# Performance work log

Hardware: AMD Instinct MI355X
Metric: run time of the kernel (lower is better)

Reference implementation:

```python
import jax, jax.numpy as jnp
import numpy as np

B, S, T, D, H, DF, E = 16, 1024, 512, 512, 8, 2048, 4
DH = D // H
EPS = 1e-5


def setup_inputs() -> dict:
    key = jax.random.key(0)
    ks = iter(jax.random.split(key, 64))

    def nrm(shape, scale=0.02):
        return jax.random.normal(next(ks), shape, dtype=jnp.float32) * scale

    inp = {
        "x": jax.random.normal(next(ks), (B, S, D), dtype=jnp.float32),
        "cross": jax.random.normal(next(ks), (B, T, D), dtype=jnp.float32),
    }
    for p in ("sa", "ca"):
        for w in ("wq", "wk", "wv", "wo"):
            inp[f"{p}_{w}"] = nrm((D, D))
            inp[f"{p}_b{w[1]}"] = jnp.zeros((D,), jnp.float32)
    inp["gate_w"] = nrm((D, E))
    inp["gate_b"] = jnp.zeros((E,), jnp.float32)
    inp["exp_w1"] = nrm((E, D, DF))
    inp["exp_b1"] = jnp.zeros((E, DF), jnp.float32)
    inp["exp_w2"] = nrm((E, DF, D))
    inp["exp_b2"] = jnp.zeros((E, D), jnp.float32)
    for i in (1, 2, 3):
        inp[f"n{i}_g"] = jnp.ones((D,), jnp.float32)
        inp[f"n{i}_b"] = jnp.zeros((D,), jnp.float32)
    return inp


def layer_norm(x, g, b):
    m = x.mean(-1, keepdims=True)
    v = x.var(-1, keepdims=True)
    return (x - m) * jax.lax.rsqrt(v + EPS) * g + b


def mha(q_in, kv_in, wq, bq, wk, bk, wv, bv, wo, bo, causal):
    Bq, Sq, _ = q_in.shape
    Sk = kv_in.shape[1]
    q = (q_in @ wq + bq).reshape(Bq, Sq, H, DH)
    k = (kv_in @ wk + bk).reshape(Bq, Sk, H, DH)
    v = (kv_in @ wv + bv).reshape(Bq, Sk, H, DH)
    scores = jnp.einsum('bshd,bthd->bhst', q, k) / jnp.sqrt(jnp.float32(DH))
    if causal:
        mask = jnp.tril(jnp.ones((Sq, Sk), dtype=bool))
        scores = jnp.where(mask, scores, jnp.float32(-1e9))
    attn = jax.nn.softmax(scores, axis=-1)
    out = jnp.einsum('bhst,bthd->bshd', attn, v).reshape(Bq, Sq, D)
    return out @ wo + bo


def moe_ffn(x, gw, gb, w1, b1, w2, b2):
    gates = jax.nn.softmax(x @ gw + gb, axis=-1)            # [B,S,E]
    h = jax.nn.relu(jnp.einsum('bsd,edf->bsef', x, w1) + b1)  # [B,S,E,DF]
    yo = jnp.einsum('bsef,efd->bsed', h, w2) + b2            # [B,S,E,D]
    y = jnp.einsum('bse,bsed->bsd', gates, yo)
    imp = gates.mean((0, 1))                                 # importance per expert
    aux = jnp.float32(E) * jnp.sum(imp * imp)                # load-balance penalty
    return y, aux


def reference(x, cross,
              sa_wq, sa_bq, sa_wk, sa_bk, sa_wv, sa_bv, sa_wo, sa_bo,
              ca_wq, ca_bq, ca_wk, ca_bk, ca_wv, ca_bv, ca_wo, ca_bo,
              gate_w, gate_b, exp_w1, exp_b1, exp_w2, exp_b2,
              n1_g, n1_b, n2_g, n2_b, n3_g, n3_b):
    # dropout is identity in eval mode
    x = x + mha(x, x, sa_wq, sa_bq, sa_wk, sa_bk, sa_wv, sa_bv, sa_wo, sa_bo, causal=True)
    x = layer_norm(x, n1_g, n1_b)
    x = x + mha(x, cross, ca_wq, ca_bq, ca_wk, ca_bk, ca_wv, ca_bv, ca_wo, ca_bo, causal=False)
    x = layer_norm(x, n2_g, n2_b)
    y, aux_loss = moe_ffn(x, gate_w, gate_b, exp_w1, exp_b1, exp_w2, exp_b2)
    out = layer_norm(x + y, n3_g, n3_b)
    return out, aux_loss
```

## Files before the change

kernel.cpp:

```cpp
#include <hip/hip_runtime.h>
#include <stdint.h>
#include <stddef.h>

typedef unsigned short bf16u;
typedef __attribute__((ext_vector_type(8))) short short8;
typedef __attribute__((ext_vector_type(4))) float f32x4;

__device__ __forceinline__ bf16u f2bf(float f) {
  union { float f; unsigned u; } v; v.f = f;
  unsigned r = v.u + 0x7FFFu + ((v.u >> 16) & 1u);
  return (bf16u)(r >> 16);
}

#define GL16(g, l) __builtin_amdgcn_global_load_lds( \
    (const __attribute__((address_space(1))) unsigned int*)(g), \
    (__attribute__((address_space(3))) unsigned int*)(l), 16, 0, 0)

enum { EPI_BF16 = 0, EPI_RELU_GATE = 1, EPI_VT = 2, EPI_RES = 3, EPI_ACC = 4 };

template<int EPI>
__global__ __launch_bounds__(256, 2) void gemm_k(
    const bf16u* __restrict__ A, const bf16u* __restrict__ BT,
    const float* __restrict__ bias, const float* __restrict__ res,
    const float* __restrict__ gates,
    bf16u* __restrict__ outb, float* __restrict__ outf,
    int M, int N, int K, int slog, int egate, int firste)
{
  __shared__ bf16u Ab[2][128 * 32];
  __shared__ bf16u Bb[2][128 * 32];
  const int tid = threadIdx.x, lane = tid & 63, w = tid >> 6;
  const int wm = w >> 1, wn = w & 1;
  const int nbt = N >> 7;
  const int mt = blockIdx.x / nbt, nt = blockIdx.x - mt * nbt;
  const int bm = mt << 7, bn = nt << 7;

  const int srow = lane >> 2;
  const int scol = (lane & 3) << 3;
  const bf16u* ap0 = A + (size_t)(bm + w * 16 + srow) * K + scol;
  const bf16u* ap1 = ap0 + (size_t)64 * K;
  const bf16u* bp0 = BT + (size_t)(bn + w * 16 + srow) * K + scol;
  const bf16u* bp1 = bp0 + (size_t)64 * K;

  f32x4 acc[4][4] = {};
  const int NT = K >> 5;

  GL16(ap0, &Ab[0][w * 512]);
  GL16(ap1, &Ab[0][(4 + w) * 512]);
  GL16(bp0, &Bb[0][w * 512]);
  GL16(bp1, &Bb[0][(4 + w) * 512]);
  __syncthreads();

  const int rl = lane & 15, kg = (lane >> 4) << 3;
  int cur = 0;
  for (int kt = 0; kt < NT; ++kt) {
    if (kt + 1 < NT) {
      const int ko = (kt + 1) << 5;
      const int nb = cur ^ 1;
      GL16(ap0 + ko, &Ab[nb][w * 512]);
      GL16(ap1 + ko, &Ab[nb][(4 + w) * 512]);
      GL16(bp0 + ko, &Bb[nb][w * 512]);
      GL16(bp1 + ko, &Bb[nb][(4 + w) * 512]);
    }
    short8 af[4], bfv[4];
    #pragma unroll
    for (int i = 0; i < 4; ++i)
      af[i] = *(const short8*)&Ab[cur][(wm * 64 + i * 16 + rl) * 32 + kg];
    #pragma unroll
    for (int j = 0; j < 4; ++j)
      bfv[j] = *(const short8*)&Bb[cur][(wn * 64 + j * 16 + rl) * 32 + kg];
    #pragma unroll
    for (int i = 0; i < 4; ++i)
      #pragma unroll
      for (int j = 0; j < 4; ++j)
        acc[i][j] = __builtin_amdgcn_mfma_f32_16x16x32_bf16(af[i], bfv[j], acc[i][j], 0, 0, 0);
    __syncthreads();
    cur ^= 1;
  }

  const int r0 = bm + wm * 64, c0 = bn + wn * 64;
  const int rsub = (lane >> 4) << 2;
  #pragma unroll
  for (int j = 0; j < 4; ++j) {
    const int col = c0 + j * 16 + rl;
    const float bs = bias ? bias[col] : 0.f;
    #pragma unroll
    for (int i = 0; i < 4; ++i) {
      const f32x4 v = acc[i][j];
      #pragma unroll
      for (int jj = 0; jj < 4; ++jj) {
        const int row = r0 + i * 16 + rsub + jj;
        float val = v[jj] + bs;
        if (EPI == EPI_BF16) {
          outb[(size_t)row * N + col] = f2bf(val);
        } else if (EPI == EPI_RELU_GATE) {
          const float g = gates[(size_t)row * 4 + egate];
          outb[(size_t)row * N + col] = f2bf(g * (val > 0.f ? val : 0.f));
        } else if (EPI == EPI_VT) {
          const int b_ = row >> slog, t_ = row & ((1 << slog) - 1);
          outb[(((size_t)(b_ * 8 + (col >> 6)) << 6) + (size_t)(col & 63)) * ((size_t)1 << slog) + t_] = f2bf(val);
        } else if (EPI == EPI_RES) {
          outf[(size_t)row * N + col] = res[(size_t)row * N + col] + val;
        } else {
          const size_t oi = (size_t)row * N + col;
          outf[oi] = firste ? val : (outf[oi] + val);
        }
      }
    }
  }
}

template<bool CAUSAL>
__global__ __launch_bounds__(256, 4) void attn_k(
    const bf16u* __restrict__ Q, const bf16u* __restrict__ Kg,
    const bf16u* __restrict__ VT, bf16u* __restrict__ O,
    int Sq, int Sk)
{
  __shared__ bf16u Kl[2][64 * 64];
  __shared__ bf16u Vl[2][64 * 64];
  __shared__ bf16u Pl[64 * 64];
  const int nqt = Sq >> 6;
  const int bh = blockIdx.x / nqt, qt = blockIdx.x - bh * nqt;
  const int b = bh >> 3, h = bh & 7;
  const int tid = threadIdx.x, lane = tid & 63, w = tid >> 6;
  const int rl = lane & 15, g4 = lane >> 4;

  const int qrow = qt * 64 + w * 16 + rl;
  const bf16u* qp = Q + (size_t)(b * Sq + qrow) * 512 + h * 64 + g4 * 8;
  const short8 qf0 = *(const short8*)qp;
  const short8 qf1 = *(const short8*)(qp + 32);

  f32x4 oacc[4] = {};
  float ml = -1e30f, ll = 0.f;
  const int KT = CAUSAL ? (qt + 1) : (Sk >> 6);

  const int str = tid >> 2, stc = tid & 3;
  const int sw_st = (str & 7) << 4;
  const bf16u* kq = Kg + (size_t)(b * Sk + str) * 512 + h * 64 + stc * 8;
  const bf16u* vq = VT + (size_t)(bh * 64 + str) * Sk + stc * 8;
  const int lo0 = str * 128 + ((stc * 16) ^ sw_st);
  const int lo1 = str * 128 + ((stc * 16 + 64) ^ sw_st);

  const int qr = w * 16 + rl;
  char* const pbase = (char*)Pl + qr * 128;
  const int swq = (qr & 7) << 4;

  {
    const short8 k0 = *(const short8*)kq;
    const short8 k1 = *(const short8*)(kq + 32);
    const short8 v0 = *(const short8*)vq;
    const short8 v1 = *(const short8*)(vq + 32);
    *(short8*)((char*)Kl[0] + lo0) = k0;
    *(short8*)((char*)Kl[0] + lo1) = k1;
    *(short8*)((char*)Vl[0] + lo0) = v0;
    *(short8*)((char*)Vl[0] + lo1) = v1;
  }
  __syncthreads();

  int cur = 0;
  for (int kt = 0; kt < KT; ++kt) {
    short8 nk0, nk1, nv0, nv1;
    const bool pre = (kt + 1 < KT);
    if (pre) {
      const bf16u* ks = kq + (size_t)(kt + 1) * 64 * 512;
      const bf16u* vs = vq + (kt + 1) * 64;
      nk0 = *(const short8*)ks;
      nk1 = *(const short8*)(ks + 32);
      nv0 = *(const short8*)vs;
      nv1 = *(const short8*)(vs + 32);
    }

    const bf16u* Kc = Kl[cur];
    const bf16u* Vc = Vl[cur];
    f32x4 st[4] = {};
    #pragma unroll
    for (int mi = 0; mi < 4; ++mi) {
      const int kr = mi * 16 + rl;
      const char* kb_ = (const char*)Kc + kr * 128;
      const int sw = (kr & 7) << 4;
      const short8 kf0 = *(const short8*)(kb_ + ((g4 * 16) ^ sw));
      const short8 kf1 = *(const short8*)(kb_ + ((g4 * 16 + 64) ^ sw));
      st[mi] = __builtin_amdgcn_mfma_f32_16x16x32_bf16(kf0, qf0, st[mi], 0, 0, 0);
      st[mi] = __builtin_amdgcn_mfma_f32_16x16x32_bf16(kf1, qf1, st[mi], 0, 0, 0);
    }

    const float SC = 0.125f * 1.44269504f;
    float sv[16];
    float pm = -1e30f;
    if (CAUSAL && kt == qt) {
      const int qg = qt * 64 + qr;
      #pragma unroll
      for (int mi = 0; mi < 4; ++mi)
        #pragma unroll
        for (int jj = 0; jj < 4; ++jj) {
          float s = st[mi][jj] * SC;
          const int kgi = kt * 64 + mi * 16 + g4 * 4 + jj;
          if (kgi > qg) s = -1e30f;
          sv[mi * 4 + jj] = s;
          pm = fmaxf(pm, s);
        }
    } else {
      #pragma unroll
      for (int mi = 0; mi < 4; ++mi)
        #pragma unroll
        for (int jj = 0; jj < 4; ++jj) {
          const float s = st[mi][jj] * SC;
          sv[mi * 4 + jj] = s;
          pm = fmaxf(pm, s);
        }
    }
    pm = fmaxf(pm, __shfl_xor(pm, 16));
    pm = fmaxf(pm, __shfl_xor(pm, 32));
    const float mnew = fmaxf(ml, pm);
    const float alpha = exp2f(ml - mnew);
    float ps = 0.f;
    bf16u pb[16];
    #pragma unroll
    for (int ii = 0; ii < 16; ++ii) {
      const float p = exp2f(sv[ii] - mnew);
      ps += p;
      pb[ii] = f2bf(p);
    }
    ps += __shfl_xor(ps, 16);
    ps += __shfl_xor(ps, 32);
    ll = ll * alpha + ps;
    ml = mnew;

    #pragma unroll
    for (int jj = 0; jj < 4; ++jj) {
      const float aj = __shfl(alpha, g4 * 4 + jj);
      #pragma unroll
      for (int ni = 0; ni < 4; ++ni) oacc[ni][jj] *= aj;
    }

    #pragma unroll
    for (int mi = 0; mi < 4; ++mi) {
      #pragma unroll
      for (int jp = 0; jp < 2; ++jp) {
        const unsigned pk = (unsigned)pb[mi * 4 + jp * 2] | ((unsigned)pb[mi * 4 + jp * 2 + 1] << 16);
        const int kx2 = mi * 32 + g4 * 8 + jp * 4;
        *(unsigned*)(pbase + (kx2 ^ swq)) = pk;
      }
    }
    asm volatile("s_waitcnt lgkmcnt(0)" ::: "memory");
    #pragma unroll
    for (int ks = 0; ks < 2; ++ks) {
      const short8 pf = *(const short8*)(pbase + ((g4 * 16 + ks * 64) ^ swq));
      #pragma unroll
      for (int ni = 0; ni < 4; ++ni) {
        const int vr = ni * 16 + rl;
        const short8 vf = *(const short8*)((const char*)Vc + vr * 128 + ((g4 * 16 + ks * 64) ^ ((vr & 7) << 4)));
        oacc[ni] = __builtin_amdgcn_mfma_f32_16x16x32_bf16(pf, vf, oacc[ni], 0, 0, 0);
      }
    }

    __syncthreads();
    if (pre) {
      const int nb = cur ^ 1;
      *(short8*)((char*)Kl[nb] + lo0) = nk0;
      *(short8*)((char*)Kl[nb] + lo1) = nk1;
      *(short8*)((char*)Vl[nb] + lo0) = nv0;
      *(short8*)((char*)Vl[nb] + lo1) = nv1;
      __syncthreads();
    }
    cur ^= 1;
  }

  #pragma unroll
  for (int jj = 0; jj < 4; ++jj) {
    const float lj = __shfl(ll, g4 * 4 + jj);
    const float inv = 1.f / lj;
    const int row = qt * 64 + w * 16 + g4 * 4 + jj;
    #pragma unroll
    for (int ni = 0; ni < 4; ++ni)
      O[(size_t)(b * Sq + row) * 512 + h * 64 + ni * 16 + rl] = f2bf(oacc[ni][jj] * inv);
  }
}

template<bool ADD, bool BOUT>
__global__ __launch_bounds__(256, 4) void ln_k(
    const float* __restrict__ X, const float* __restrict__ Y,
    const float* __restrict__ gam, const float* __restrict__ bet,
    float* __restrict__ outf, bf16u* __restrict__ outb)
{
  const int row = blockIdx.x * 4 + (threadIdx.x >> 6);
  const int lane = threadIdx.x & 63;
  const float* xp = X + (size_t)row * 512 + lane * 8;
  float v[8];
  {
    const float4 t0 = *(const float4*)xp;
    const float4 t1 = *(const float4*)(xp + 4);
    v[0] = t0.x; v[1] = t0.y; v[2] = t0.z; v[3] = t0.w;
    v[4] = t1.x; v[5] = t1.y; v[6] = t1.z; v[7] = t1.w;
  }
  if (ADD) {
    const float* yp = Y + (size_t)row * 512 + lane * 8;
    const float4 t0 = *(const float4*)yp;
    const float4 t1 = *(const float4*)(yp + 4);
    v[0] += t0.x; v[1] += t0.y; v[2] += t0.z; v[3] += t0.w;
    v[4] += t1.x; v[5] += t1.y; v[6] += t1.z; v[7] += t1.w;
  }
  float s = 0.f, q = 0.f;
  #pragma unroll
  for (int i = 0; i < 8; ++i) { s += v[i]; q += v[i] * v[i]; }
  #pragma unroll
  for (int off = 1; off < 64; off <<= 1) {
    s += __shfl_xor(s, off);
    q += __shfl_xor(q, off);
  }
  const float mean = s * (1.f / 512.f);
  const float var = q * (1.f / 512.f) - mean * mean;
  const float rs = rsqrtf(var + 1e-5f);
  float o[8];
  #pragma unroll
  for (int i = 0; i < 8; ++i) {
    const float g = gam[lane * 8 + i], bb = bet[lane * 8 + i];
    o[i] = (v[i] - mean) * rs * g + bb;
  }
  float* op = outf + (size_t)row * 512 + lane * 8;
  *(float4*)op = make_float4(o[0], o[1], o[2], o[3]);
  *(float4*)(op + 4) = make_float4(o[4], o[5], o[6], o[7]);
  if (BOUT) {
    union { bf16u u[8]; short8 v8; } pk;
    #pragma unroll
    for (int i = 0; i < 8; ++i) pk.u[i] = f2bf(o[i]);
    *(short8*)(outb + (size_t)row * 512 + lane * 8) = pk.v8;
  }
}

__global__ __launch_bounds__(256, 4) void ln_final_k(
    const float* __restrict__ X, const float* __restrict__ Y,
    const float* __restrict__ gates, const float* __restrict__ b2,
    const float* __restrict__ gam, const float* __restrict__ bet,
    float* __restrict__ outf)
{
  const int row = blockIdx.x * 4 + (threadIdx.x >> 6);
  const int lane = threadIdx.x & 63;
  const float4 gv4 = *(const float4*)(gates + (size_t)row * 4);
  float v[8];
  {
    const float* xp = X + (size_t)row * 512 + lane * 8;
    const float* yp = Y + (size_t)row * 512 + lane * 8;
    const float4 t0 = *(const float4*)xp;
    const float4 t1 = *(const float4*)(xp + 4);
    const float4 u0 = *(const float4*)yp;
    const float4 u1 = *(const float4*)(yp + 4);
    v[0] = t0.x + u0.x; v[1] = t0.y + u0.y; v[2] = t0.z + u0.z; v[3] = t0.w + u0.w;
    v[4] = t1.x + u1.x; v[5] = t1.y + u1.y; v[6] = t1.z + u1.z; v[7] = t1.w + u1.w;
  }
  #pragma unroll
  for (int e = 0; e < 4; ++e) {
    const float ge = e == 0 ? gv4.x : e == 1 ? gv4.y : e == 2 ? gv4.z : gv4.w;
    const float4 b0 = *(const float4*)(b2 + e * 512 + lane * 8);
    const float4 b1 = *(const float4*)(b2 + e * 512 + lane * 8 + 4);
    v[0] += ge * b0.x; v[1] += ge * b0.y; v[2] += ge * b0.z; v[3] += ge * b0.w;
    v[4] += ge * b1.x; v[5] += ge * b1.y; v[6] += ge * b1.z; v[7] += ge * b1.w;
  }
  float s = 0.f, q = 0.f;
  #pragma unroll
  for (int i = 0; i < 8; ++i) { s += v[i]; q += v[i] * v[i]; }
  #pragma unroll
  for (int off = 1; off < 64; off <<= 1) {
    s += __shfl_xor(s, off);
    q += __shfl_xor(q, off);
  }
  const float mean = s * (1.f / 512.f);
  const float var = q * (1.f / 512.f) - mean * mean;
  const float rs = rsqrtf(var + 1e-5f);
  float* op = outf + (size_t)row * 512 + lane * 8;
  float o[8];
  #pragma unroll
  for (int i = 0; i < 8; ++i)
    o[i] = (v[i] - mean) * rs * gam[lane * 8 + i] + bet[lane * 8 + i];
  *(float4*)op = make_float4(o[0], o[1], o[2], o[3]);
  *(float4*)(op + 4) = make_float4(o[4], o[5], o[6], o[7]);
}

__global__ __launch_bounds__(256, 4) void gate_k(
    const float* __restrict__ X, const float* __restrict__ gw,
    const float* __restrict__ gb, float* __restrict__ gates,
    float* __restrict__ imp)
{
  __shared__ float sh[4];
  const int tid = threadIdx.x;
  if (tid < 4) sh[tid] = 0.f;
  __syncthreads();
  const int row = blockIdx.x * 4 + (tid >> 6);
  const int lane = tid & 63;
  const float* xr = X + (size_t)row * 512;
  float a0 = 0.f, a1 = 0.f, a2 = 0.f, a3 = 0.f;
  for (int d = lane; d < 512; d += 64) {
    const float xv = xr[d];
    const float4 wv = *(const float4*)(gw + d * 4);
    a0 += xv * wv.x; a1 += xv * wv.y; a2 += xv * wv.z; a3 += xv * wv.w;
  }
  #pragma unroll
  for (int off = 1; off < 64; off <<= 1) {
    a0 += __shfl_xor(a0, off); a1 += __shfl_xor(a1, off);
    a2 += __shfl_xor(a2, off); a3 += __shfl_xor(a3, off);
  }
  if (lane == 0) {
    a0 += gb[0]; a1 += gb[1]; a2 += gb[2]; a3 += gb[3];
    const float m = fmaxf(fmaxf(a0, a1), fmaxf(a2, a3));
    const float e0 = exp2f((a0 - m) * 1.44269504f);
    const float e1 = exp2f((a1 - m) * 1.44269504f);
    const float e2 = exp2f((a2 - m) * 1.44269504f);
    const float e3 = exp2f((a3 - m) * 1.44269504f);
    const float inv = 1.f / (e0 + e1 + e2 + e3);
    float* gr = gates + (size_t)row * 4;
    const float g0 = e0 * inv, g1 = e1 * inv, g2 = e2 * inv, g3 = e3 * inv;
    gr[0] = g0; gr[1] = g1; gr[2] = g2; gr[3] = g3;
    atomicAdd(&sh[0], g0); atomicAdd(&sh[1], g1);
    atomicAdd(&sh[2], g2); atomicAdd(&sh[3], g3);
  }
  __syncthreads();
  if (tid < 4) atomicAdd(&imp[tid], sh[tid]);
}

__global__ void aux_k(const float* __restrict__ imp, float* __restrict__ out) {
  if (threadIdx.x == 0 && blockIdx.x == 0) {
    float s = 0.f;
    #pragma unroll
    for (int e = 0; e < 4; ++e) { const float v = imp[e] * (1.f / 16384.f); s += v * v; }
    out[0] = 4.f * s;
  }
}

__global__ __launch_bounds__(256, 4) void conv_k(const float* __restrict__ in, bf16u* __restrict__ out) {
  const size_t i = ((size_t)blockIdx.x * 256 + threadIdx.x) * 8;
  const float4 a = *(const float4*)(in + i);
  const float4 b = *(const float4*)(in + i + 4);
  union { bf16u u[8]; short8 v; } pk;
  pk.u[0] = f2bf(a.x); pk.u[1] = f2bf(a.y); pk.u[2] = f2bf(a.z); pk.u[3] = f2bf(a.w);
  pk.u[4] = f2bf(b.x); pk.u[5] = f2bf(b.y); pk.u[6] = f2bf(b.z); pk.u[7] = f2bf(b.w);
  *(short8*)(out + i) = pk.v;
}

__global__ __launch_bounds__(256, 4) void trans_k(
    const float* __restrict__ W, bf16u* __restrict__ WT, int K, int N)
{
  __shared__ float t[32][33];
  const int tx = threadIdx.x & 31, ty = threadIdx.x >> 5;
  const int n0 = blockIdx.x * 32, k0 = blockIdx.y * 32;
  #pragma unroll
  for (int i = 0; i < 4; ++i)
    t[ty + i * 8][tx] = W[(size_t)(k0 + ty + i * 8) * N + n0 + tx];
  __syncthreads();
  #pragma unroll
  for (int i = 0; i < 4; ++i)
    WT[(size_t)(n0 + ty + i * 8) * K + k0 + tx] = f2bf(t[tx][ty + i * 8]);
}

extern "C" void kernel_launch(void* const* d_in, const int* in_sizes, int n_in,
                              void* d_out, int out_size, void* d_ws, size_t ws_size,
                              hipStream_t stream)
{
  const int B = 16, S = 1024, T = 512, D = 512, DF = 2048, E = 4;
  const int M = B * S;
  const int Mc = B * T;
  (void)in_sizes; (void)n_in; (void)out_size; (void)ws_size;

  const float* x      = (const float*)d_in[0];
  const float* cross  = (const float*)d_in[1];
  const float* gate_w = (const float*)d_in[18];
  const float* gate_b = (const float*)d_in[19];
  const float* exp_w1 = (const float*)d_in[20];
  const float* exp_b1 = (const float*)d_in[21];
  const float* exp_w2 = (const float*)d_in[22];
  const float* exp_b2 = (const float*)d_in[23];

  char* p = (char*)d_ws;
  auto alloc = [&](size_t bytes) -> char* {
    char* r = p;
    p += (bytes + 255) & ~(size_t)255;
    return r;
  };
  bf16u* xb    = (bf16u*)alloc((size_t)M * D * 2);
  bf16u* crb   = (bf16u*)alloc((size_t)Mc * D * 2);
  bf16u* wT    = (bf16u*)alloc((size_t)8 * D * D * 2);
  bf16u* w1T   = (bf16u*)alloc((size_t)E * DF * D * 2);
  bf16u* w2T   = (bf16u*)alloc((size_t)E * D * DF * 2);
  bf16u* qb    = (bf16u*)alloc((size_t)M * D * 2);
  bf16u* kb    = (bf16u*)alloc((size_t)M * D * 2);
  bf16u* vTb   = (bf16u*)alloc((size_t)M * D * 2);
  bf16u* ao    = (bf16u*)alloc((size_t)M * D * 2);
  float* xf    = (float*)alloc((size_t)M * D * 4);
  bf16u* x2b   = (bf16u*)alloc((size_t)M * D * 2);
  float* gates = (float*)alloc((size_t)M * 4 * 4);
  float* imp   = (float*)alloc(256);
  bf16u* hbuf  = (bf16u*)alloc((size_t)M * DF * 2);
  float* y     = (float*)alloc((size_t)M * D * 4);

  hipMemsetAsync(imp, 0, 32, stream);
  conv_k<<<(M * D) / 2048, 256, 0, stream>>>(x, xb);
  conv_k<<<(Mc * D) / 2048, 256, 0, stream>>>(cross, crb);
  for (int i = 0; i < 8; ++i)
    trans_k<<<dim3(D / 32, D / 32), 256, 0, stream>>>((const float*)d_in[2 + 2 * i], wT + (size_t)i * D * D, D, D);
  for (int e = 0; e < E; ++e)
    trans_k<<<dim3(DF / 32, D / 32), 256, 0, stream>>>(exp_w1 + (size_t)e * D * DF, w1T + (size_t)e * DF * D, D, DF);
  for (int e = 0; e < E; ++e)
    trans_k<<<dim3(D / 32, DF / 32), 256, 0, stream>>>(exp_w2 + (size_t)e * DF * D, w2T + (size_t)e * D * DF, DF, D);

  const int gMD  = (M / 128) * (D / 128);
  const int gMcD = (Mc / 128) * (D / 128);
  const int gMDF = (M / 128) * (DF / 128);

  gemm_k<EPI_BF16><<<gMD, 256, 0, stream>>>(xb, wT + 0 * (size_t)D * D, (const float*)d_in[3], nullptr, nullptr, qb, nullptr, M, D, D, 0, 0, 0);
  gemm_k<EPI_BF16><<<gMD, 256, 0, stream>>>(xb, wT + 1 * (size_t)D * D, (const float*)d_in[5], nullptr, nullptr, kb, nullptr, M, D, D, 0, 0, 0);
  gemm_k<EPI_VT><<<gMD, 256, 0, stream>>>(xb, wT + 2 * (size_t)D * D, (const float*)d_in[7], nullptr, nullptr, vTb, nullptr, M, D, D, 10, 0, 0);
  attn_k<true><<<B * 8 * (S / 64), 256, 0, stream>>>(qb, kb, vTb, ao, S, S);
  gemm_k<EPI_RES><<<gMD, 256, 0, stream>>>(ao, wT + 3 * (size_t)D * D, (const float*)d_in[9], x, nullptr, nullptr, xf, M, D, D, 0, 0, 0);
  ln_k<false, true><<<M / 4, 256, 0, stream>>>(xf, nullptr, (const float*)d_in[24], (const float*)d_in[25], xf, x2b);

  gemm_k<EPI_BF16><<<gMD, 256, 0, stream>>>(x2b, wT + 4 * (size_t)D * D, (const float*)d_in[11], nullptr, nullptr, qb, nullptr, M, D, D, 0, 0, 0);
  gemm_k<EPI_BF16><<<gMcD, 256, 0, stream>>>(crb, wT + 5 * (size_t)D * D, (const float*)d_in[13], nullptr, nullptr, kb, nullptr, Mc, D, D, 0, 0, 0);
  gemm_k<EPI_VT><<<gMcD, 256, 0, stream>>>(crb, wT + 6 * (size_t)D * D, (const float*)d_in[15], nullptr, nullptr, vTb, nullptr, Mc, D, D, 9, 0, 0);
  attn_k<false><<<B * 8 * (S / 64), 256, 0, stream>>>(qb, kb, vTb, ao, S, T);
  gemm_k<EPI_RES><<<gMD, 256, 0, stream>>>(ao, wT + 7 * (size_t)D * D, (const float*)d_in[17], xf, nullptr, nullptr, xf, M, D, D, 0, 0, 0);
  ln_k<false, true><<<M / 4, 256, 0, stream>>>(xf, nullptr, (const float*)d_in[26], (const float*)d_in[27], xf, x2b);

  gate_k<<<M / 4, 256, 0, stream>>>(xf, gate_w, gate_b, gates, imp);
  aux_k<<<1, 64, 0, stream>>>(imp, (float*)d_out + (size_t)M * D);
  for (int e = 0; e < E; ++e) {
    gemm_k<EPI_RELU_GATE><<<gMDF, 256, 0, stream>>>(x2b, w1T + (size_t)e * DF * D, exp_b1 + (size_t)e * DF, nullptr, gates, hbuf, nullptr, M, DF, D, 0, e, 0);
    gemm_k<EPI_ACC><<<gMD, 256, 0, stream>>>(hbuf, w2T + (size_t)e * D * DF, nullptr, nullptr, nullptr, nullptr, y, M, D, DF, 0, 0, e == 0 ? 1 : 0);
  }
  ln_final_k<<<M / 4, 256, 0, stream>>>(xf, y, gates, exp_b2, (const float*)d_in[28], (const float*)d_in[29], (float*)d_out);
}
```

Before: 1.010 ms.

## Process 128 query rows per attention block, read K/V from global, remap block ids

The attention kernel now handles two 64-row query tiles per block, sharing each K and V fragment between both tiles. It drops the LDS double-buffered K/V staging and block-wide barriers, loading K and V fragments straight from global memory, which relies on cache hits instead. It also packs probabilities with v_cvt_pk_bf16_f32. Both the GEMM and attention kernels remap block ids across 8 groups, presumably to spread neighbouring tiles over XCDs for better L2 locality. In exchange, register pressure rises (launch bounds lowered to 3 blocks) and the attention grid is halved.

```diff
diff --git a/kernel.cpp b/kernel.cpp
--- a/kernel.cpp
+++ b/kernel.cpp
@@ -30,8 +30,10 @@
   __shared__ bf16u Bb[2][128 * 32];
   const int tid = threadIdx.x, lane = tid & 63, w = tid >> 6;
   const int wm = w >> 1, wn = w & 1;
+  const int cpx = gridDim.x >> 3;
+  const int bid = (blockIdx.x & 7) * cpx + (blockIdx.x >> 3);
   const int nbt = N >> 7;
-  const int mt = blockIdx.x / nbt, nt = blockIdx.x - mt * nbt;
+  const int mt = bid / nbt, nt = bid - mt * nbt;
   const int bm = mt << 7, bn = nt << 7;
 
   const int srow = lane >> 2;
@@ -109,170 +111,135 @@
   }
 }
 
+#define SOFTMAX_G(stv, mlv, llv, oaccv, pbX, DOMASK, QG)                     \
+  {                                                                          \
+    float sv[16]; float pm = -1e30f;                                         \
+    _Pragma("unroll")                                                        \
+    for (int mi = 0; mi < 4; ++mi) {                                         \
+      _Pragma("unroll")                                                      \
+      for (int jj = 0; jj < 4; ++jj) {                                       \
+        float s_ = stv[mi][jj] * SC;                                         \
+        if (DOMASK) {                                                        \
+          const int kgi = kt * 64 + mi * 16 + g4 * 4 + jj;                   \
+          if (kgi > (QG)) s_ = -1e30f;                                       \
+        }                                                                    \
+        sv[mi * 4 + jj] = s_; pm = fmaxf(pm, s_);                            \
+      }                                                                      \
+    }                                                                        \
+    pm = fmaxf(pm, __shfl_xor(pm, 16));                                      \
+    pm = fmaxf(pm, __shfl_xor(pm, 32));                                      \
+    const float mnew = fmaxf(mlv, pm);                                       \
+    const float alpha = exp2f(mlv - mnew);                                   \
+    float ps = 0.f;                                                          \
+    _Pragma("unroll")                                                        \
+    for (int mi = 0; mi < 4; ++mi) {                                         \
+      const float p0_ = exp2f(sv[mi * 4 + 0] - mnew);                        \
+      const float p1_ = exp2f(sv[mi * 4 + 1] - mnew);                        \
+      const float p2_ = exp2f(sv[mi * 4 + 2] - mnew);                        \
+      const float p3_ = exp2f(sv[mi * 4 + 3] - mnew);                        \
+      ps += (p0_ + p1_) + (p2_ + p3_);                                       \
+      unsigned w0_, w1_;                                                     \
+      asm("v_cvt_pk_bf16_f32 %0, %1, %2" : "=v"(w0_) : "v"(p0_), "v"(p1_)); \
+      asm("v_cvt_pk_bf16_f32 %0, %1, %2" : "=v"(w1_) : "v"(p2_), "v"(p3_)); \
+      *(unsigned*)(pbX + ((mi * 32 + g4 * 8 + 0) ^ swq)) = w0_;              \
+      *(unsigned*)(pbX + ((mi * 32 + g4 * 8 + 4) ^ swq)) = w1_;              \
+    }                                                                        \
+    ps += __shfl_xor(ps, 16);                                                \
+    ps += __shfl_xor(ps, 32);                                                \
+    llv = llv * alpha + ps; mlv = mnew;                                      \
+    _Pragma("unroll")                                                        \
+    for (int jj = 0; jj < 4; ++jj) {                                         \
+      const float aj = __shfl(alpha, g4 * 4 + jj);                           \
+      _Pragma("unroll")                                                      \
+      for (int ni = 0; ni < 4; ++ni) oaccv[ni][jj] *= aj;                    \
+    }                                                                        \
+  }
+
 template<bool CAUSAL>
-__global__ __launch_bounds__(256, 4) void attn_k(
+__global__ __launch_bounds__(256, 3) void attn_k(
     const bf16u* __restrict__ Q, const bf16u* __restrict__ Kg,
     const bf16u* __restrict__ VT, bf16u* __restrict__ O,
     int Sq, int Sk)
 {
-  __shared__ bf16u Kl[2][64 * 64];
-  __shared__ bf16u Vl[2][64 * 64];
-  __shared__ bf16u Pl[64 * 64];
-  const int nqt = Sq >> 6;
-  const int bh = blockIdx.x / nqt, qt = blockIdx.x - bh * nqt;
+  __shared__ bf16u Pl[128 * 64];
+  const int nqt = Sq >> 7;
+  const int cpx = gridDim.x >> 3;
+  const int bid = (blockIdx.x & 7) * cpx + (blockIdx.x >> 3);
+  const int bh = bid / nqt, qt = bid - bh * nqt;
   const int b = bh >> 3, h = bh & 7;
   const int tid = threadIdx.x, lane = tid & 63, w = tid >> 6;
   const int rl = lane & 15, g4 = lane >> 4;
 
-  const int qrow = qt * 64 + w * 16 + rl;
-  const bf16u* qp = Q + (size_t)(b * Sq + qrow) * 512 + h * 64 + g4 * 8;
-  const short8 qf0 = *(const short8*)qp;
-  const short8 qf1 = *(const short8*)(qp + 32);
-
-  f32x4 oacc[4] = {};
-  float ml = -1e30f, ll = 0.f;
-  const int KT = CAUSAL ? (qt + 1) : (Sk >> 6);
-
-  const int str = tid >> 2, stc = tid & 3;
-  const int sw_st = (str & 7) << 4;
-  const bf16u* kq = Kg + (size_t)(b * Sk + str) * 512 + h * 64 + stc * 8;
-  const bf16u* vq = VT + (size_t)(bh * 64 + str) * Sk + stc * 8;
-  const int lo0 = str * 128 + ((stc * 16) ^ sw_st);
-  const int lo1 = str * 128 + ((stc * 16 + 64) ^ sw_st);
-
   const int qr = w * 16 + rl;
-  char* const pbase = (char*)Pl + qr * 128;
+  const int qbase = qt * 128;
+
+  const bf16u* qp0 = Q + (size_t)(b * Sq + qbase + qr) * 512 + h * 64 + g4 * 8;
+  const bf16u* qp1 = qp0 + (size_t)64 * 512;
+  const short8 qa0 = *(const short8*)qp0;
+  const short8 qa1 = *(const short8*)(qp0 + 32);
+  const short8 qc0 = *(const short8*)qp1;
+  const short8 qc1 = *(const short8*)(qp1 + 32);
+
+  f32x4 oacc0[4] = {}, oacc1[4] = {};
+  float ml0 = -1e30f, ll0 = 0.f, ml1 = -1e30f, ll1 = 0.f;
+  const int KT = CAUSAL ? (2 * qt + 2) : (Sk >> 6);
+
+  const bf16u* kbase = Kg + (size_t)b * Sk * 512 + h * 64;
+  const bf16u* vbase = VT + (size_t)bh * 64 * Sk;
+
+  char* const pb0 = (char*)Pl + qr * 128;
+  char* const pb1 = (char*)Pl + (64 + qr) * 128;
   const int swq = (qr & 7) << 4;
-
-  {
-    const short8 k0 = *(const short8*)kq;
-    const short8 k1 = *(const short8*)(kq + 32);
-    const short8 v0 = *(const short8*)vq;
-    const short8 v1 = *(const short8*)(vq + 32);
-    *(short8*)((char*)Kl[0] + lo0) = k0;
-    *(short8*)((char*)Kl[0] + lo1) = k1;
-    *(short8*)((char*)Vl[0] + lo0) = v0;
-    *(short8*)((char*)Vl[0] + lo1) = v1;
-  }
-  __syncthreads();
-
-  int cur = 0;
+  const float SC = 0.125f * 1.44269504f;
+
   for (int kt = 0; kt < KT; ++kt) {
-    short8 nk0, nk1, nv0, nv1;
-    const bool pre = (kt + 1 < KT);
-    if (pre) {
-      const bf16u* ks = kq + (size_t)(kt + 1) * 64 * 512;
-      const bf16u* vs = vq + (kt + 1) * 64;
-      nk0 = *(const short8*)ks;
-      nk1 = *(const short8*)(ks + 32);
-      nv0 = *(const short8*)vs;
-      nv1 = *(const short8*)(vs + 32);
+    const bool mask0 = CAUSAL && (kt == 2 * qt);
+    const bool skip0 = CAUSAL && (kt == 2 * qt + 1);
+    const bool mask1 = CAUSAL && (kt == 2 * qt + 1);
+
+    f32x4 st0[4] = {}, st1[4] = {};
+    #pragma unroll
+    for (int mi = 0; mi < 4; ++mi) {
+      const bf16u* kp = kbase + (size_t)(kt * 64 + mi * 16 + rl) * 512 + g4 * 8;
+      const short8 kf0 = *(const short8*)kp;
+      const short8 kf1 = *(const short8*)(kp + 32);
+      if (!skip0) {
+        st0[mi] = __builtin_amdgcn_mfma_f32_16x16x32_bf16(kf0, qa0, st0[mi], 0, 0, 0);
+        st0[mi] = __builtin_amdgcn_mfma_f32_16x16x32_bf16(kf1, qa1, st0[mi], 0, 0, 0);
+      }
+      st1[mi] = __builtin_amdgcn_mfma_f32_16x16x32_bf16(kf0, qc0, st1[mi], 0, 0, 0);
+      st1[mi] = __builtin_amdgcn_mfma_f32_16x16x32_bf16(kf1, qc1, st1[mi], 0, 0, 0);
     }
 
-    const bf16u* Kc = Kl[cur];
-    const bf16u* Vc = Vl[cur];
-    f32x4 st[4] = {};
-    #pragma unroll
-    for (int mi = 0; mi < 4; ++mi) {
-      const int kr = mi * 16 + rl;
-      const char* kb_ = (const char*)Kc + kr * 128;
-      const int sw = (kr & 7) << 4;
-      const short8 kf0 = *(const short8*)(kb_ + ((g4 * 16) ^ sw));
-      const short8 kf1 = *(const short8*)(kb_ + ((g4 * 16 + 64) ^ sw));
-      st[mi] = __builtin_amdgcn_mfma_f32_16x16x32_bf16(kf0, qf0, st[mi], 0, 0, 0);
-      st[mi] = __builtin_amdgcn_mfma_f32_16x16x32_bf16(kf1, qf1, st[mi], 0, 0, 0);
-    }
-
-    const float SC = 0.125f * 1.44269504f;
-    float sv[16];
-    float pm = -1e30f;
-    if (CAUSAL && kt == qt) {
-      const int qg = qt * 64 + qr;
+    if (!skip0) SOFTMAX_G(st0, ml0, ll0, oacc0, pb0, mask0, qbase + qr);
+    SOFTMAX_G(st1, ml1, ll1, oacc1, pb1, mask1, qbase + 64 + qr);
+
+    asm volatile("s_waitcnt lgkmcnt(0)" ::: "memory");
+
+    #pragma unroll
+    for (int ks = 0; ks < 2; ++ks) {
+      const short8 pf0 = *(const short8*)(pb0 + ((g4 * 16 + ks * 64) ^ swq));
+      const short8 pf1 = *(const short8*)(pb1 + ((g4 * 16 + ks * 64) ^ swq));
       #pragma unroll
-      for (int mi = 0; mi < 4; ++mi)
-        #pragma unroll
-        for (int jj = 0; jj < 4; ++jj) {
-          float s = st[mi][jj] * SC;
-          const int kgi = kt * 64 + mi * 16 + g4 * 4 + jj;
-          if (kgi > qg) s = -1e30f;
-          sv[mi * 4 + jj] = s;
-          pm = fmaxf(pm, s);
-        }
-    } else {
-      #pragma unroll
-      for (int mi = 0; mi < 4; ++mi)
-        #pragma unroll
-        for (int jj = 0; jj < 4; ++jj) {
-          const float s = st[mi][jj] * SC;
-          sv[mi * 4 + jj] = s;
-          pm = fmaxf(pm, s);
-        }
-    }
-    pm = fmaxf(pm, __shfl_xor(pm, 16));
-    pm = fmaxf(pm, __shfl_xor(pm, 32));
-    const float mnew = fmaxf(ml, pm);
-    const float alpha = exp2f(ml - mnew);
-    float ps = 0.f;
-    bf16u pb[16];
-    #pragma unroll
-    for (int ii = 0; ii < 16; ++ii) {
-      const float p = exp2f(sv[ii] - mnew);
-      ps += p;
-      pb[ii] = f2bf(p);
-    }
-    ps += __shfl_xor(ps, 16);
-    ps += __shfl_xor(ps, 32);
-    ll = ll * alpha + ps;
-    ml = mnew;
-
-    #pragma unroll
-    for (int jj = 0; jj < 4; ++jj) {
-      const float aj = __shfl(alpha, g4 * 4 + jj);
-      #pragma unroll
-      for (int ni = 0; ni < 4; ++ni) oacc[ni][jj] *= aj;
-    }
-
-    #pragma unroll
-    for (int mi = 0; mi < 4; ++mi) {
-      #pragma unroll
-      for (int jp = 0; jp < 2; ++jp) {
-        const unsigned pk = (unsigned)pb[mi * 4 + jp * 2] | ((unsigned)pb[mi * 4 + jp * 2 + 1] << 16);
-        const int kx2 = mi * 32 + g4 * 8 + jp * 4;
-        *(unsigned*)(pbase + (kx2 ^ swq)) = pk;
+      for (int ni = 0; ni < 4; ++ni) {
+        const short8 vf = *(const short8*)(vbase + (size_t)(ni * 16 + rl) * Sk + kt * 64 + ks * 32 + g4 * 8);
+        if (!skip0) oacc0[ni] = __builtin_amdgcn_mfma_f32_16x16x32_bf16(pf0, vf, oacc0[ni], 0, 0, 0);
+        oacc1[ni] = __builtin_amdgcn_mfma_f32_16x16x32_bf16(pf1, vf, oacc1[ni], 0, 0, 0);
       }
     }
-    asm volatile("s_waitcnt lgkmcnt(0)" ::: "memory");
-    #pragma unroll
-    for (int ks = 0; ks < 2; ++ks) {
-      const short8 pf = *(const short8*)(pbase + ((g4 * 16 + ks * 64) ^ swq));
-      #pragma unroll
-      for (int ni = 0; ni < 4; ++ni) {
-        const int vr = ni * 16 + rl;
-        const short8 vf = *(const short8*)((const char*)Vc + vr * 128 + ((g4 * 16 + ks * 64) ^ ((vr & 7) << 4)));
-        oacc[ni] = __builtin_amdgcn_mfma_f32_16x16x32_bf16(pf, vf, oacc[ni], 0, 0, 0);
-      }
+  }
+
+  #pragma unroll
+  for (int jj = 0; jj < 4; ++jj) {
+    const float l0 = __shfl(ll0, g4 * 4 + jj);
+    const float l1 = __shfl(ll1, g4 * 4 + jj);
+    const float i0 = 1.f / l0, i1 = 1.f / l1;
+    const int row0 = qbase + w * 16 + g4 * 4 + jj;
+    #pragma unroll
+    for (int ni = 0; ni < 4; ++ni) {
+      O[(size_t)(b * Sq + row0) * 512 + h * 64 + ni * 16 + rl] = f2bf(oacc0[ni][jj] * i0);
+      O[(size_t)(b * Sq + row0 + 64) * 512 + h * 64 + ni * 16 + rl] = f2bf(oacc1[ni][jj] * i1);
     }
-
-    __syncthreads();
-    if (pre) {
-      const int nb = cur ^ 1;
-      *(short8*)((char*)Kl[nb] + lo0) = nk0;
-      *(short8*)((char*)Kl[nb] + lo1) = nk1;
-      *(short8*)((char*)Vl[nb] + lo0) = nv0;
-      *(short8*)((char*)Vl[nb] + lo1) = nv1;
-      __syncthreads();
-    }
-    cur ^= 1;
-  }
-
-  #pragma unroll
-  for (int jj = 0; jj < 4; ++jj) {
-    const float lj = __shfl(ll, g4 * 4 + jj);
-    const float inv = 1.f / lj;
-    const int row = qt * 64 + w * 16 + g4 * 4 + jj;
-    #pragma unroll
-    for (int ni = 0; ni < 4; ++ni)
-      O[(size_t)(b * Sq + row) * 512 + h * 64 + ni * 16 + rl] = f2bf(oacc[ni][jj] * inv);
   }
 }
 
@@ -503,18 +470,19 @@
   const int gMD  = (M / 128) * (D / 128);
   const int gMcD = (Mc / 128) * (D / 128);
   const int gMDF = (M / 128) * (DF / 128);
+  const int gATT = B * 8 * (S / 128);
 
   gemm_k<EPI_BF16><<<gMD, 256, 0, stream>>>(xb, wT + 0 * (size_t)D * D, (const float*)d_in[3], nullptr, nullptr, qb, nullptr, M, D, D, 0, 0, 0);
   gemm_k<EPI_BF16><<<gMD, 256, 0, stream>>>(xb, wT + 1 * (size_t)D * D, (const float*)d_in[5], nullptr, nullptr, kb, nullptr, M, D, D, 0, 0, 0);
   gemm_k<EPI_VT><<<gMD, 256, 0, stream>>>(xb, wT + 2 * (size_t)D * D, (const float*)d_in[7], nullptr, nullptr, vTb, nullptr, M, D, D, 10, 0, 0);
-  attn_k<true><<<B * 8 * (S / 64), 256, 0, stream>>>(qb, kb, vTb, ao, S, S);
+  attn_k<true><<<gATT, 256, 0, stream>>>(qb, kb, vTb, ao, S, S);
   gemm_k<EPI_RES><<<gMD, 256, 0, stream>>>(ao, wT + 3 * (size_t)D * D, (const float*)d_in[9], x, nullptr, nullptr, xf, M, D, D, 0, 0, 0);
   ln_k<false, true><<<M / 4, 256, 0, stream>>>(xf, nullptr, (const float*)d_in[24], (const float*)d_in[25], xf, x2b);
 
   gemm_k<EPI_BF16><<<gMD, 256, 0, stream>>>(x2b, wT + 4 * (size_t)D * D, (const float*)d_in[11], nullptr, nullptr, qb, nullptr, M, D, D, 0, 0, 0);
   gemm_k<EPI_BF16><<<gMcD, 256, 0, stream>>>(crb, wT + 5 * (size_t)D * D, (const float*)d_in[13], nullptr, nullptr, kb, nullptr, Mc, D, D, 0, 0, 0);
   gemm_k<EPI_VT><<<gMcD, 256, 0, stream>>>(crb, wT + 6 * (size_t)D * D, (const float*)d_in[15], nullptr, nullptr, vTb, nullptr, Mc, D, D, 9, 0, 0);
-  attn_k<false><<<B * 8 * (S / 64), 256, 0, stream>>>(qb, kb, vTb, ao, S, T);
+  attn_k<false><<<gATT, 256, 0, stream>>>(qb, kb, vTb, ao, S, T);
   gemm_k<EPI_RES><<<gMD, 256, 0, stream>>>(ao, wT + 7 * (size_t)D * D, (const float*)d_in[17], xf, nullptr, nullptr, xf, M, D, D, 0, 0, 0);
   ln_k<false, true><<<M / 4, 256, 0, stream>>>(xf, nullptr, (const float*)d_in[26], (const float*)d_in[27], xf, x2b);
 
```

Measured after the change: 1.047 ms. +3.7%, slower.

## Replace GEMM with 256-row swizzled double-buffered kernel and fuse QKV projections

Applied to the files above, without the earlier changes.

Replaces the 128x128 GEMM with a 512-thread kernel that computes 256xBN tiles with a K-step of 64. It uses XOR-swizzled LDS layout, a two-stage prefetch with explicit vmcnt waits and s_setprio around the MFMA blocks, and an XCD-aware block remap. The Q/K/V projections of self-attention are fused into one N=1536 GEMM, and the cross-attention K/V into one N=1024 GEMM, using concatenated bias buffers. The aim is more data reuse per LDS load, fewer bank conflicts and fewer launches. The cost is higher register and LDS pressure per block and a hardcoded assumption that the transposed weights are laid out contiguously.

```diff
diff --git a/kernel.cpp b/kernel.cpp
--- a/kernel.cpp
+++ b/kernel.cpp
@@ -16,93 +16,157 @@
     (const __attribute__((address_space(1))) unsigned int*)(g), \
     (__attribute__((address_space(3))) unsigned int*)(l), 16, 0, 0)
 
-enum { EPI_BF16 = 0, EPI_RELU_GATE = 1, EPI_VT = 2, EPI_RES = 3, EPI_ACC = 4 };
-
-template<int EPI>
-__global__ __launch_bounds__(256, 2) void gemm_k(
+enum { EPI_BF16 = 0, EPI_RELU_GATE = 1, EPI_QKV = 2, EPI_RES = 3, EPI_ACC = 4, EPI_KV = 5 };
+
+template<int EPI, int BN>
+__global__ __launch_bounds__(512, 2) void gemm256(
     const bf16u* __restrict__ A, const bf16u* __restrict__ BT,
     const float* __restrict__ bias, const float* __restrict__ res,
     const float* __restrict__ gates,
-    bf16u* __restrict__ outb, float* __restrict__ outf,
-    int M, int N, int K, int slog, int egate, int firste)
+    bf16u* __restrict__ o1, bf16u* __restrict__ o2, bf16u* __restrict__ o3,
+    float* __restrict__ of,
+    int N, int K, int LDA, int LDB, int slog, int egate, int firste)
 {
-  __shared__ bf16u Ab[2][128 * 32];
-  __shared__ bf16u Bb[2][128 * 32];
+  constexpr int NI = BN / 64;
+  constexpr int NB = BN / 64;
+  constexpr int LOADS = 4 + NB;
+  __shared__ bf16u Al[2][256 * 64];
+  __shared__ bf16u Bl[2][BN * 64];
+
   const int tid = threadIdx.x, lane = tid & 63, w = tid >> 6;
-  const int wm = w >> 1, wn = w & 1;
-  const int nbt = N >> 7;
-  const int mt = blockIdx.x / nbt, nt = blockIdx.x - mt * nbt;
-  const int bm = mt << 7, bn = nt << 7;
-
-  const int srow = lane >> 2;
-  const int scol = (lane & 3) << 3;
-  const bf16u* ap0 = A + (size_t)(bm + w * 16 + srow) * K + scol;
-  const bf16u* ap1 = ap0 + (size_t)64 * K;
-  const bf16u* bp0 = BT + (size_t)(bn + w * 16 + srow) * K + scol;
-  const bf16u* bp1 = bp0 + (size_t)64 * K;
-
-  f32x4 acc[4][4] = {};
-  const int NT = K >> 5;
-
-  GL16(ap0, &Ab[0][w * 512]);
-  GL16(ap1, &Ab[0][(4 + w) * 512]);
-  GL16(bp0, &Bb[0][w * 512]);
-  GL16(bp1, &Bb[0][(4 + w) * 512]);
-  __syncthreads();
-
-  const int rl = lane & 15, kg = (lane >> 4) << 3;
+  const int wm = w >> 2, wn = w & 3;
+  const int rl = lane & 15, g4 = lane >> 4, rsub = g4 * 4;
+
+  const int cpx = gridDim.x >> 3;
+  const int bid = (blockIdx.x & 7) * cpx + (blockIdx.x >> 3);
+  const int nbt = N / BN;
+  const int mt = bid / nbt, nt = bid - mt * nbt;
+  const int bm = mt * 256, bn = nt * BN;
+
+  const int lrow = lane >> 3;
+  const int lcol = ((lane & 7) * 8) ^ (lrow * 8);
+
+  auto stage = [&](int buf, int kt) {
+    const int ko = kt * 64 + lcol;
+    #pragma unroll
+    for (int i = 0; i < 4; ++i) {
+      const int r = i * 64 + w * 8;
+      GL16(A + (size_t)(bm + r + lrow) * LDA + ko, &Al[buf][r * 64]);
+    }
+    #pragma unroll
+    for (int i = 0; i < NB; ++i) {
+      const int r = i * 64 + w * 8;
+      GL16(BT + (size_t)(bn + r + lrow) * LDB + ko, &Bl[buf][r * 64]);
+    }
+  };
+
+  f32x4 acc[8][NI] = {};
+  const int NT = K >> 6;
+
+  stage(0, 0);
+  stage(1, 1);
+  asm volatile("s_waitcnt vmcnt(%0)" :: "n"(LOADS) : "memory");
+  __builtin_amdgcn_sched_barrier(0);
+  __builtin_amdgcn_s_barrier();
+  __builtin_amdgcn_sched_barrier(0);
+
   int cur = 0;
   for (int kt = 0; kt < NT; ++kt) {
+    short8 a0[8], b0[NI];
+    #pragma unroll
+    for (int mi = 0; mi < 8; ++mi) {
+      const int r = wm * 128 + mi * 16 + rl;
+      a0[mi] = *(const short8*)&Al[cur][r * 64 + ((g4 * 8) ^ ((r & 7) * 8))];
+    }
+    #pragma unroll
+    for (int ni = 0; ni < NI; ++ni) {
+      const int r = wn * (NI * 16) + ni * 16 + rl;
+      b0[ni] = *(const short8*)&Bl[cur][r * 64 + ((g4 * 8) ^ ((r & 7) * 8))];
+    }
+    __builtin_amdgcn_s_setprio(1);
+    #pragma unroll
+    for (int mi = 0; mi < 8; ++mi)
+      #pragma unroll
+      for (int ni = 0; ni < NI; ++ni)
+        acc[mi][ni] = __builtin_amdgcn_mfma_f32_16x16x32_bf16(a0[mi], b0[ni], acc[mi][ni], 0, 0, 0);
+    __builtin_amdgcn_s_setprio(0);
+
+    short8 a1[8], b1[NI];
+    #pragma unroll
+    for (int mi = 0; mi < 8; ++mi) {
+      const int r = wm * 128 + mi * 16 + rl;
+      a1[mi] = *(const short8*)&Al[cur][r * 64 + ((32 + g4 * 8) ^ ((r & 7) * 8))];
+    }
+    #pragma unroll
+    for (int ni = 0; ni < NI; ++ni) {
+      const int r = wn * (NI * 16) + ni * 16 + rl;
+      b1[ni] = *(const short8*)&Bl[cur][r * 64 + ((32 + g4 * 8) ^ ((r & 7) * 8))];
+    }
+    asm volatile("s_waitcnt lgkmcnt(0)" ::: "memory");
+    __builtin_amdgcn_sched_barrier(0);
+    __builtin_amdgcn_s_barrier();
+    __builtin_amdgcn_sched_barrier(0);
+
+    if (kt + 2 < NT) stage(cur, kt + 2);
+
+    __builtin_amdgcn_s_setprio(1);
+    #pragma unroll
+    for (int mi = 0; mi < 8; ++mi)
+      #pragma unroll
+      for (int ni = 0; ni < NI; ++ni)
+        acc[mi][ni] = __builtin_amdgcn_mfma_f32_16x16x32_bf16(a1[mi], b1[ni], acc[mi][ni], 0, 0, 0);
+    __builtin_amdgcn_s_setprio(0);
+
     if (kt + 1 < NT) {
-      const int ko = (kt + 1) << 5;
-      const int nb = cur ^ 1;
-      GL16(ap0 + ko, &Ab[nb][w * 512]);
-      GL16(ap1 + ko, &Ab[nb][(4 + w) * 512]);
-      GL16(bp0 + ko, &Bb[nb][w * 512]);
-      GL16(bp1 + ko, &Bb[nb][(4 + w) * 512]);
-    }
-    short8 af[4], bfv[4];
-    #pragma unroll
-    for (int i = 0; i < 4; ++i)
-      af[i] = *(const short8*)&Ab[cur][(wm * 64 + i * 16 + rl) * 32 + kg];
-    #pragma unroll
-    for (int j = 0; j < 4; ++j)
-      bfv[j] = *(const short8*)&Bb[cur][(wn * 64 + j * 16 + rl) * 32 + kg];
-    #pragma unroll
-    for (int i = 0; i < 4; ++i)
-      #pragma unroll
-      for (int j = 0; j < 4; ++j)
-        acc[i][j] = __builtin_amdgcn_mfma_f32_16x16x32_bf16(af[i], bfv[j], acc[i][j], 0, 0, 0);
-    __syncthreads();
+      if (kt + 2 < NT) {
+        asm volatile("s_waitcnt vmcnt(%0)" :: "n"(LOADS) : "memory");
+      } else {
+        asm volatile("s_waitcnt vmcnt(0)" ::: "memory");
+      }
+      __builtin_amdgcn_sched_barrier(0);
+      __builtin_amdgcn_s_barrier();
+      __builtin_amdgcn_sched_barrier(0);
+    }
     cur ^= 1;
   }
 
-  const int r0 = bm + wm * 64, c0 = bn + wn * 64;
-  const int rsub = (lane >> 4) << 2;
-  #pragma unroll
-  for (int j = 0; j < 4; ++j) {
-    const int col = c0 + j * 16 + rl;
+  const int r0 = bm + wm * 128, c0 = bn + wn * (NI * 16);
+  #pragma unroll
+  for (int ni = 0; ni < NI; ++ni) {
+    const int col = c0 + ni * 16 + rl;
     const float bs = bias ? bias[col] : 0.f;
     #pragma unroll
-    for (int i = 0; i < 4; ++i) {
-      const f32x4 v = acc[i][j];
+    for (int mi = 0; mi < 8; ++mi) {
+      const f32x4 v = acc[mi][ni];
       #pragma unroll
       for (int jj = 0; jj < 4; ++jj) {
-        const int row = r0 + i * 16 + rsub + jj;
-        float val = v[jj] + bs;
+        const int row = r0 + mi * 16 + rsub + jj;
+        const float val = v[jj] + bs;
         if (EPI == EPI_BF16) {
-          outb[(size_t)row * N + col] = f2bf(val);
+          o1[(size_t)row * N + col] = f2bf(val);
         } else if (EPI == EPI_RELU_GATE) {
           const float g = gates[(size_t)row * 4 + egate];
-          outb[(size_t)row * N + col] = f2bf(g * (val > 0.f ? val : 0.f));
-        } else if (EPI == EPI_VT) {
-          const int b_ = row >> slog, t_ = row & ((1 << slog) - 1);
-          outb[(((size_t)(b_ * 8 + (col >> 6)) << 6) + (size_t)(col & 63)) * ((size_t)1 << slog) + t_] = f2bf(val);
+          o1[(size_t)row * N + col] = f2bf(g * (val > 0.f ? val : 0.f));
+        } else if (EPI == EPI_QKV) {
+          if (col < 512) o1[(size_t)row * 512 + col] = f2bf(val);
+          else if (col < 1024) o2[(size_t)row * 512 + col - 512] = f2bf(val);
+          else {
+            const int c = col - 1024;
+            const int b_ = row >> slog, t_ = row & ((1 << slog) - 1);
+            o3[(((size_t)(b_ * 8 + (c >> 6)) << 6) + (size_t)(c & 63)) * ((size_t)1 << slog) + t_] = f2bf(val);
+          }
+        } else if (EPI == EPI_KV) {
+          if (col < 512) o2[(size_t)row * 512 + col] = f2bf(val);
+          else {
+            const int c = col - 512;
+            const int b_ = row >> slog, t_ = row & ((1 << slog) - 1);
+            o3[(((size_t)(b_ * 8 + (c >> 6)) << 6) + (size_t)(c & 63)) * ((size_t)1 << slog) + t_] = f2bf(val);
+          }
         } else if (EPI == EPI_RES) {
-          outf[(size_t)row * N + col] = res[(size_t)row * N + col] + val;
+          of[(size_t)row * N + col] = res[(size_t)row * N + col] + val;
         } else {
           const size_t oi = (size_t)row * N + col;
-          outf[oi] = firste ? val : (outf[oi] + val);
+          of[oi] = firste ? val : (of[oi] + val);
         }
       }
     }
@@ -489,8 +553,16 @@
   float* imp   = (float*)alloc(256);
   bf16u* hbuf  = (bf16u*)alloc((size_t)M * DF * 2);
   float* y     = (float*)alloc((size_t)M * D * 4);
+  float* qkvb  = (float*)alloc(1536 * 4);
+  float* kvb   = (float*)alloc(1024 * 4);
 
   hipMemsetAsync(imp, 0, 32, stream);
+  hipMemcpyAsync(qkvb,        d_in[3], 512 * 4, hipMemcpyDeviceToDevice, stream);
+  hipMemcpyAsync(qkvb + 512,  d_in[5], 512 * 4, hipMemcpyDeviceToDevice, stream);
+  hipMemcpyAsync(qkvb + 1024, d_in[7], 512 * 4, hipMemcpyDeviceToDevice, stream);
+  hipMemcpyAsync(kvb,         d_in[13], 512 * 4, hipMemcpyDeviceToDevice, stream);
+  hipMemcpyAsync(kvb + 512,   d_in[15], 512 * 4, hipMemcpyDeviceToDevice, stream);
+
   conv_k<<<(M * D) / 2048, 256, 0, stream>>>(x, xb);
   conv_k<<<(Mc * D) / 2048, 256, 0, stream>>>(cross, crb);
   for (int i = 0; i < 8; ++i)
@@ -500,29 +572,37 @@
   for (int e = 0; e < E; ++e)
     trans_k<<<dim3(D / 32, DF / 32), 256, 0, stream>>>(exp_w2 + (size_t)e * DF * D, w2T + (size_t)e * D * DF, DF, D);
 
-  const int gMD  = (M / 128) * (D / 128);
-  const int gMcD = (Mc / 128) * (D / 128);
-  const int gMDF = (M / 128) * (DF / 128);
-
-  gemm_k<EPI_BF16><<<gMD, 256, 0, stream>>>(xb, wT + 0 * (size_t)D * D, (const float*)d_in[3], nullptr, nullptr, qb, nullptr, M, D, D, 0, 0, 0);
-  gemm_k<EPI_BF16><<<gMD, 256, 0, stream>>>(xb, wT + 1 * (size_t)D * D, (const float*)d_in[5], nullptr, nullptr, kb, nullptr, M, D, D, 0, 0, 0);
-  gemm_k<EPI_VT><<<gMD, 256, 0, stream>>>(xb, wT + 2 * (size_t)D * D, (const float*)d_in[7], nullptr, nullptr, vTb, nullptr, M, D, D, 10, 0, 0);
-  attn_k<true><<<B * 8 * (S / 64), 256, 0, stream>>>(qb, kb, vTb, ao, S, S);
-  gemm_k<EPI_RES><<<gMD, 256, 0, stream>>>(ao, wT + 3 * (size_t)D * D, (const float*)d_in[9], x, nullptr, nullptr, xf, M, D, D, 0, 0, 0);
+  const int gATT = B * 8 * (S / 64);
+
+  gemm256<EPI_QKV, 256><<<(M / 256) * 6, 512, 0, stream>>>(
+      xb, wT, qkvb, nullptr, nullptr, qb, kb, vTb, nullptr, 1536, 512, 512, 512, 10, 0, 0);
+  attn_k<true><<<gATT, 256, 0, stream>>>(qb, kb, vTb, ao, S, S);
+  gemm256<EPI_RES, 128><<<(M / 256) * 4, 512, 0, stream>>>(
+      ao, wT + 3 * (size_t)D * D, (const float*)d_in[9], x, nullptr,
+      nullptr, nullptr, nullptr, xf, 512, 512, 512, 512, 0, 0, 0);
   ln_k<false, true><<<M / 4, 256, 0, stream>>>(xf, nullptr, (const float*)d_in[24], (const float*)d_in[25], xf, x2b);
 
-  gemm_k<EPI_BF16><<<gMD, 256, 0, stream>>>(x2b, wT + 4 * (size_t)D * D, (const float*)d_in[11], nullptr, nullptr, qb, nullptr, M, D, D, 0, 0, 0);
-  gemm_k<EPI_BF16><<<gMcD, 256, 0, stream>>>(crb, wT + 5 * (size_t)D * D, (const float*)d_in[13], nullptr, nullptr, kb, nullptr, Mc, D, D, 0, 0, 0);
-  gemm_k<EPI_VT><<<gMcD, 256, 0, stream>>>(crb, wT + 6 * (size_t)D * D, (const float*)d_in[15], nullptr, nullptr, vTb, nullptr, Mc, D, D, 9, 0, 0);
-  attn_k<false><<<B * 8 * (S / 64), 256, 0, stream>>>(qb, kb, vTb, ao, S, T);
-  gemm_k<EPI_RES><<<gMD, 256, 0, stream>>>(ao, wT + 7 * (size_t)D * D, (const float*)d_in[17], xf, nullptr, nullptr, xf, M, D, D, 0, 0, 0);
+  gemm256<EPI_BF16, 128><<<(M / 256) * 4, 512, 0, stream>>>(
+      x2b, wT + 4 * (size_t)D * D, (const float*)d_in[11], nullptr, nullptr,
+      qb, nullptr, nullptr, nullptr, 512, 512, 512, 512, 0, 0, 0);
+  gemm256<EPI_KV, 128><<<(Mc / 256) * 8, 512, 0, stream>>>(
+      crb, wT + 5 * (size_t)D * D, kvb, nullptr, nullptr,
+      nullptr, kb, vTb, nullptr, 1024, 512, 512, 512, 9, 0, 0);
+  attn_k<false><<<gATT, 256, 0, stream>>>(qb, kb, vTb, ao, S, T);
+  gemm256<EPI_RES, 128><<<(M / 256) * 4, 512, 0, stream>>>(
+      ao, wT + 7 * (size_t)D * D, (const float*)d_in[17], xf, nullptr,
+      nullptr, nullptr, nullptr, xf, 512, 512, 512, 512, 0, 0, 0);
   ln_k<false, true><<<M / 4, 256, 0, stream>>>(xf, nullptr, (const float*)d_in[26], (const float*)d_in[27], xf, x2b);
 
   gate_k<<<M / 4, 256, 0, stream>>>(xf, gate_w, gate_b, gates, imp);
   aux_k<<<1, 64, 0, stream>>>(imp, (float*)d_out + (size_t)M * D);
   for (int e = 0; e < E; ++e) {
-    gemm_k<EPI_RELU_GATE><<<gMDF, 256, 0, stream>>>(x2b, w1T + (size_t)e * DF * D, exp_b1 + (size_t)e * DF, nullptr, gates, hbuf, nullptr, M, DF, D, 0, e, 0);
-    gemm_k<EPI_ACC><<<gMD, 256, 0, stream>>>(hbuf, w2T + (size_t)e * D * DF, nullptr, nullptr, nullptr, nullptr, y, M, D, DF, 0, 0, e == 0 ? 1 : 0);
+    gemm256<EPI_RELU_GATE, 256><<<(M / 256) * 8, 512, 0, stream>>>(
+        x2b, w1T + (size_t)e * DF * D, exp_b1 + (size_t)e * DF, nullptr, gates,
+        hbuf, nullptr, nullptr, nullptr, 2048, 512, 512, 512, 0, e, 0);
+    gemm256<EPI_ACC, 128><<<(M / 256) * 4, 512, 0, stream>>>(
+        hbuf, w2T + (size_t)e * D * DF, nullptr, nullptr, nullptr,
+        nullptr, nullptr, nullptr, y, 512, 2048, 2048, 2048, 0, 0, e == 0 ? 1 : 0);
   }
   ln_final_k<<<M / 4, 256, 0, stream>>>(xf, y, gates, exp_b2, (const float*)d_in[28], (const float*)d_in[29], (float*)d_out);
 }
```

Result: slower. 1.062 ms (+5.2%).
